# Performance work log

Measured on AMD Instinct MI355X. Metric: run time of the kernel, lower is better.

Reference implementation:

```python
import jax, jax.numpy as jnp
import numpy as np


def setup_inputs() -> dict:
    key = jax.random.key(0)
    k1, k2, k3, k4 = jax.random.split(key, 4)
    B, S, D, E, C = 8, 128, 480, 8, 10
    gcn_outputs = jax.random.normal(k1, (B, S, D), dtype=jnp.float32)
    label_sm = jax.random.uniform(k2, (B, S, S, C), dtype=jnp.float32)
    weight_prob = jax.random.uniform(k3, (B, S, S, E), dtype=jnp.float32)
    tensor_masks = jnp.ones((B, S, S), dtype=bool)
    # Linear(994, 10) with xavier-uniform weight
    fan_in, fan_out = 994, C
    bound = float(np.sqrt(6.0 / (fan_in + fan_out)))
    W_weight = jax.random.uniform(k4, (C, 994), dtype=jnp.float32, minval=-bound, maxval=bound)
    W_bias = jnp.zeros((C,), dtype=jnp.float32)
    return {"gcn_outputs": gcn_outputs, "label_sm": label_sm,
            "weight_prob": weight_prob, "tensor_masks": tensor_masks,
            "W_weight": W_weight, "W_bias": W_bias}


def reference(gcn_outputs, label_sm, weight_prob, tensor_masks, W_weight, W_bias):
    B, S, D = gcn_outputs.shape
    # node1[b,i,j,:] = node[b,j]; node2[b,i,j,:] = node[b,i]
    node1 = jnp.broadcast_to(gcn_outputs[:, None, :, :], (B, S, S, D))
    node2 = jnp.broadcast_to(gcn_outputs[:, :, None, :], (B, S, S, D))
    # edge_diag[b,s,e] = weight_prob[b,s,s,e]
    edge_diag = jnp.diagonal(weight_prob, axis1=1, axis2=2).transpose(0, 2, 1)  # [B,S,E]
    E = edge_diag.shape[-1]
    edge_i = jnp.broadcast_to(edge_diag[:, None, :, :], (B, S, S, E))  # varies along j
    edge_j = jnp.broadcast_to(edge_diag[:, :, None, :], (B, S, S, E))  # varies along i
    # channel 0 untouched, channels 1:4 upper-triangular, channels 4: lower-triangular
    mask_u = jnp.triu(jnp.ones((S, S), dtype=label_sm.dtype))[None, :, :, None]
    mask_l = jnp.tril(jnp.ones((S, S), dtype=label_sm.dtype))[None, :, :, None]
    s_triu = jnp.concatenate([
        label_sm[..., 0:1],
        label_sm[..., 1:4] * mask_u,
        label_sm[..., 4:] * mask_l,
    ], axis=-1)
    feats = jnp.concatenate([node1, node2, edge_i, edge_j, weight_prob, s_triu], axis=-1)  # [B,S,S,994]
    pre = jnp.einsum('bijf,kf->bijk', feats, W_weight) + W_bias
    return pre
```

## Files before the change

### kernel.cpp

```cpp
#include <hip/hip_runtime.h>
#include <hip/hip_bf16.h>

#define BB 8
#define SS 128
#define DD 480
#define EE 8
#define CC 10
#define KK 10
#define FF 994

__device__ __forceinline__ float cvt(float x) { return x; }
__device__ __forceinline__ float cvt(__hip_bfloat16 x) { return __bfloat162float(x); }
__device__ __forceinline__ void stf(float* p, float v) { *p = v; }
__device__ __forceinline__ void stf(__hip_bfloat16* p, float v) { *p = __float2bfloat16(v); }

__global__ __launch_bounds__(64) void detect_kernel(const unsigned short* __restrict__ wp_raw,
                                                    int* __restrict__ flag) {
    int bad = 0;
    #pragma unroll
    for (int q = 0; q < 4; ++q) {
        unsigned short v = wp_raw[threadIdx.x + 64 * q];
        if (((v >> 7) & 0xFF) >= 128) bad = 1;
    }
    unsigned long long m = __ballot(bad);
    if (threadIdx.x == 0) *flag = (m != 0ULL) ? 1 : 0;
}

template <typename T>
__device__ void rows_body(const T* __restrict__ gcn, const T* __restrict__ wp,
                          const T* __restrict__ W, const T* __restrict__ bias,
                          float* __restrict__ Arow, float* __restrict__ Brow,
                          float* g) {
    const int row = blockIdx.x;
    const int s   = row & (SS - 1);

    for (int d = threadIdx.x; d < DD; d += 256)
        g[d] = cvt(gcn[(size_t)row * DD + d]);
    __syncthreads();

    const int wave = threadIdx.x >> 6;
    const int lane = threadIdx.x & 63;
    const T* wpd = wp + ((size_t)row * SS + s) * EE;

    for (int q = 0; q < 5; ++q) {
        const int t   = wave * 5 + q;
        const int k   = (t < KK) ? t : t - KK;
        const int off = (t < KK) ? 0 : DD;
        const T* wrow = W + (size_t)k * FF + off;

        float acc = 0.f;
        for (int d = lane; d < DD; d += 64)
            acc += g[d] * cvt(wrow[d]);
        #pragma unroll
        for (int o = 32; o > 0; o >>= 1)
            acc += __shfl_down(acc, o, 64);

        if (lane == 0) {
            const int ecol = (t < KK) ? (2 * DD) : (2 * DD + EE);
            float e = 0.f;
            #pragma unroll
            for (int ee = 0; ee < EE; ++ee)
                e += cvt(wpd[ee]) * cvt(W[(size_t)k * FF + ecol + ee]);
            const float r = acc + e;
            if (t < KK) Arow[row * KK + k] = r;
            else        Brow[row * KK + k] = r + cvt(bias[k]);
        }
    }
}

__global__ __launch_bounds__(256) void rows_kernel(
    const void* gcn, const void* wp, const void* W, const void* bias,
    const int* __restrict__ flag, float* Arow, float* Brow) {
    __shared__ float g[DD];
    if (*flag)
        rows_body<float>((const float*)gcn, (const float*)wp,
                         (const float*)W, (const float*)bias, Arow, Brow, g);
    else
        rows_body<__hip_bfloat16>((const __hip_bfloat16*)gcn, (const __hip_bfloat16*)wp,
                                  (const __hip_bfloat16*)W, (const __hip_bfloat16*)bias,
                                  Arow, Brow, g);
}

template <typename T>
__device__ void pixel_body(const T* __restrict__ label, const T* __restrict__ wp,
                           const T* __restrict__ W, const float* __restrict__ Arow,
                           const float* __restrict__ Brow, T* __restrict__ out,
                           float (*w5)[EE], float (*w6)[CC], float* brow) {
    const int bi = blockIdx.x;
    const int b  = bi >> 7;
    const int i  = bi & (SS - 1);
    const int j  = threadIdx.x;

    for (int t = threadIdx.x; t < KK * EE + KK * CC + KK; t += 128) {
        if (t < KK * EE) {
            const int k = t / EE, e = t % EE;
            w5[k][e] = cvt(W[(size_t)k * FF + 2 * DD + 2 * EE + e]);
        } else if (t < KK * EE + KK * CC) {
            const int tt = t - KK * EE;
            const int k = tt / CC, c = tt % CC;
            w6[k][c] = cvt(W[(size_t)k * FF + 2 * DD + 3 * EE + c]);
        } else {
            const int k = t - KK * EE - KK * CC;
            brow[k] = Brow[bi * KK + k];
        }
    }
    __syncthreads();

    const size_t pix = (size_t)bi * SS + j;

    float wpe[EE];
    #pragma unroll
    for (int e = 0; e < EE; ++e) wpe[e] = cvt(wp[pix * EE + e]);
    float lc[CC];
    #pragma unroll
    for (int c = 0; c < CC; ++c) lc[c] = cvt(label[pix * CC + c]);

    const float mu = (j >= i) ? 1.f : 0.f;
    const float ml = (j <= i) ? 1.f : 0.f;
    #pragma unroll
    for (int c = 1; c < 4; ++c) lc[c] *= mu;
    #pragma unroll
    for (int c = 4; c < CC; ++c) lc[c] *= ml;

    const float* ap = Arow + ((size_t)b * SS + j) * KK;

    #pragma unroll
    for (int k = 0; k < KK; ++k) {
        float acc = ap[k] + brow[k];
        #pragma unroll
        for (int e = 0; e < EE; ++e) acc += wpe[e] * w5[k][e];
        #pragma unroll
        for (int c = 0; c < CC; ++c) acc += lc[c] * w6[k][c];
        stf(&out[pix * KK + k], acc);
    }
}

__global__ __launch_bounds__(128) void pixel_kernel(
    const void* label, const void* wp, const void* W,
    const float* __restrict__ Arow, const float* __restrict__ Brow,
    const int* __restrict__ flag, void* out) {
    __shared__ float w5[KK][EE];
    __shared__ float w6[KK][CC];
    __shared__ float brow[KK];
    if (*flag)
        pixel_body<float>((const float*)label, (const float*)wp, (const float*)W,
                          Arow, Brow, (float*)out, w5, w6, brow);
    else
        pixel_body<__hip_bfloat16>((const __hip_bfloat16*)label, (const __hip_bfloat16*)wp,
                                   (const __hip_bfloat16*)W, Arow, Brow,
                                   (__hip_bfloat16*)out, w5, w6, brow);
}

extern "C" void kernel_launch(void* const* d_in, const int* in_sizes, int n_in,
                              void* d_out, int out_size, void* d_ws, size_t ws_size,
                              hipStream_t stream) {
    const void* gcn   = d_in[0];
    const void* label = d_in[1];
    const void* wp    = d_in[2];
    const void* W     = d_in[4];
    const void* bias  = d_in[5];

    int*   flag = (int*)d_ws;
    float* Arow = (float*)((char*)d_ws + 256);
    float* Brow = Arow + BB * SS * KK;

    detect_kernel<<<1, 64, 0, stream>>>((const unsigned short*)wp, flag);
    rows_kernel<<<BB * SS, 256, 0, stream>>>(gcn, wp, W, bias, flag, Arow, Brow);
    pixel_kernel<<<BB * SS, 128, 0, stream>>>(label, wp, W, Arow, Brow, flag, d_out);
}
```

Measured before the change: 84.17 us.

## Drop dtype detection kernel, vectorize loads/stores, and process two rows per pixel block

Removes the bf16/fp32 detection kernel and its runtime flag branch, so both kernels are specialized to fp32 and one launch disappears. The row kernel now uses float4 loads for node features and float2 loads for weights. The pixel kernel handles two i-rows per 256-thread block, stages the per-batch Arow table in shared memory, and uses vectorized float4/float2 loads and float2 stores. The aim is to cut launch overhead and improve memory coalescing. In exchange it drops bf16 input support and relies on alignment assumptions for the vector accesses.

```diff
diff --git a/kernel.cpp b/kernel.cpp
--- a/kernel.cpp
+++ b/kernel.cpp
@@ -1,5 +1,4 @@
 #include <hip/hip_runtime.h>
-#include <hip/hip_bf16.h>
 
 #define BB 8
 #define SS 128
@@ -9,111 +8,116 @@
 #define KK 10
 #define FF 994
 
-__device__ __forceinline__ float cvt(float x) { return x; }
-__device__ __forceinline__ float cvt(__hip_bfloat16 x) { return __bfloat162float(x); }
-__device__ __forceinline__ void stf(float* p, float v) { *p = v; }
-__device__ __forceinline__ void stf(__hip_bfloat16* p, float v) { *p = __float2bfloat16(v); }
 
-__global__ __launch_bounds__(64) void detect_kernel(const unsigned short* __restrict__ wp_raw,
-                                                    int* __restrict__ flag) {
-    int bad = 0;
-    #pragma unroll
-    for (int q = 0; q < 4; ++q) {
-        unsigned short v = wp_raw[threadIdx.x + 64 * q];
-        if (((v >> 7) & 0xFF) >= 128) bad = 1;
-    }
-    unsigned long long m = __ballot(bad);
-    if (threadIdx.x == 0) *flag = (m != 0ULL) ? 1 : 0;
-}
-
-template <typename T>
-__device__ void rows_body(const T* __restrict__ gcn, const T* __restrict__ wp,
-                          const T* __restrict__ W, const T* __restrict__ bias,
-                          float* __restrict__ Arow, float* __restrict__ Brow,
-                          float* g) {
+__global__ __launch_bounds__(256) void rows_kernel(
+    const float* __restrict__ gcn,
+    const float* __restrict__ wp,
+    const float* __restrict__ W,
+    const float* __restrict__ bias,
+    float* __restrict__ Arow,
+    float* __restrict__ Brow)
+{
+    __shared__ float g[DD];
     const int row = blockIdx.x;
     const int s   = row & (SS - 1);
 
-    for (int d = threadIdx.x; d < DD; d += 256)
-        g[d] = cvt(gcn[(size_t)row * DD + d]);
+    const float4* g4 = reinterpret_cast<const float4*>(gcn + (size_t)row * DD);
+    for (int t = threadIdx.x; t < DD / 4; t += 256) {
+        const float4 v = g4[t];
+        g[4 * t + 0] = v.x; g[4 * t + 1] = v.y;
+        g[4 * t + 2] = v.z; g[4 * t + 3] = v.w;
+    }
     __syncthreads();
 
     const int wave = threadIdx.x >> 6;
     const int lane = threadIdx.x & 63;
-    const T* wpd = wp + ((size_t)row * SS + s) * EE;
 
     for (int q = 0; q < 5; ++q) {
         const int t   = wave * 5 + q;
         const int k   = (t < KK) ? t : t - KK;
         const int off = (t < KK) ? 0 : DD;
-        const T* wrow = W + (size_t)k * FF + off;
+        const float2* w2 = reinterpret_cast<const float2*>(W + (size_t)k * FF + off);
 
         float acc = 0.f;
-        for (int d = lane; d < DD; d += 64)
-            acc += g[d] * cvt(wrow[d]);
+        #pragma unroll
+        for (int r = 0; r < 4; ++r) {
+            const int idx = lane + 64 * r;
+            if (idx < DD / 2) {
+                const float2 u = w2[idx];
+                acc += g[2 * idx] * u.x + g[2 * idx + 1] * u.y;
+            }
+        }
         #pragma unroll
         for (int o = 32; o > 0; o >>= 1)
             acc += __shfl_down(acc, o, 64);
 
         if (lane == 0) {
-            const int ecol = (t < KK) ? (2 * DD) : (2 * DD + EE);
+            const float* wpd = wp + ((size_t)row * SS + s) * EE;
+            const float* we  = W + (size_t)k * FF + ((t < KK) ? 2 * DD : 2 * DD + EE);
             float e = 0.f;
             #pragma unroll
             for (int ee = 0; ee < EE; ++ee)
-                e += cvt(wpd[ee]) * cvt(W[(size_t)k * FF + ecol + ee]);
+                e += wpd[ee] * we[ee];
             const float r = acc + e;
             if (t < KK) Arow[row * KK + k] = r;
-            else        Brow[row * KK + k] = r + cvt(bias[k]);
+            else        Brow[row * KK + k] = r + bias[k];
         }
     }
 }
 
-__global__ __launch_bounds__(256) void rows_kernel(
-    const void* gcn, const void* wp, const void* W, const void* bias,
-    const int* __restrict__ flag, float* Arow, float* Brow) {
-    __shared__ float g[DD];
-    if (*flag)
-        rows_body<float>((const float*)gcn, (const float*)wp,
-                         (const float*)W, (const float*)bias, Arow, Brow, g);
-    else
-        rows_body<__hip_bfloat16>((const __hip_bfloat16*)gcn, (const __hip_bfloat16*)wp,
-                                  (const __hip_bfloat16*)W, (const __hip_bfloat16*)bias,
-                                  Arow, Brow, g);
-}
+__global__ __launch_bounds__(256) void pixel_kernel(
+    const float* __restrict__ label,
+    const float* __restrict__ wp,
+    const float* __restrict__ W,
+    const float* __restrict__ Arow,
+    const float* __restrict__ Brow,
+    float* __restrict__ out)
+{
+    const int b  = blockIdx.x >> 6;
+    const int i0 = (blockIdx.x & 63) * 2;
 
-template <typename T>
-__device__ void pixel_body(const T* __restrict__ label, const T* __restrict__ wp,
-                           const T* __restrict__ W, const float* __restrict__ Arow,
-                           const float* __restrict__ Brow, T* __restrict__ out,
-                           float (*w5)[EE], float (*w6)[CC], float* brow) {
-    const int bi = blockIdx.x;
-    const int b  = bi >> 7;
-    const int i  = bi & (SS - 1);
-    const int j  = threadIdx.x;
+    __shared__ float w5[KK][EE];
+    __shared__ float w6[KK][CC];
+    __shared__ float brow[2][KK];
+    __shared__ float arow[SS][KK + 1];
 
-    for (int t = threadIdx.x; t < KK * EE + KK * CC + KK; t += 128) {
-        if (t < KK * EE) {
-            const int k = t / EE, e = t % EE;
-            w5[k][e] = cvt(W[(size_t)k * FF + 2 * DD + 2 * EE + e]);
-        } else if (t < KK * EE + KK * CC) {
-            const int tt = t - KK * EE;
-            const int k = tt / CC, c = tt % CC;
-            w6[k][c] = cvt(W[(size_t)k * FF + 2 * DD + 3 * EE + c]);
-        } else {
-            const int k = t - KK * EE - KK * CC;
-            brow[k] = Brow[bi * KK + k];
+    {
+        const int t = threadIdx.x;
+        if (t < 80) {
+            w5[t >> 3][t & 7] = W[(t >> 3) * FF + 2 * DD + 2 * EE + (t & 7)];
+        } else if (t < 180) {
+            const int tt = t - 80;
+            w6[tt / 10][tt % 10] = W[(tt / 10) * FF + 2 * DD + 3 * EE + (tt % 10)];
+        } else if (t < 200) {
+            const int tt = t - 180;
+            brow[tt / 10][tt % 10] = Brow[(b * SS + i0 + tt / 10) * KK + (tt % 10)];
         }
     }
+    for (int u = threadIdx.x; u < SS * KK; u += 256)
+        arow[u / KK][u % KK] = Arow[(size_t)b * SS * KK + u];
     __syncthreads();
 
-    const size_t pix = (size_t)bi * SS + j;
+    const int half = threadIdx.x >> 7;
+    const int i    = i0 + half;
+    const int j    = threadIdx.x & 127;
+    const size_t pix = ((size_t)(b * SS + i)) * SS + j;
 
     float wpe[EE];
-    #pragma unroll
-    for (int e = 0; e < EE; ++e) wpe[e] = cvt(wp[pix * EE + e]);
+    {
+        const float4* p4 = reinterpret_cast<const float4*>(wp + pix * EE);
+        const float4 a = p4[0], c = p4[1];
+        wpe[0] = a.x; wpe[1] = a.y; wpe[2] = a.z; wpe[3] = a.w;
+        wpe[4] = c.x; wpe[5] = c.y; wpe[6] = c.z; wpe[7] = c.w;
+    }
     float lc[CC];
-    #pragma unroll
-    for (int c = 0; c < CC; ++c) lc[c] = cvt(label[pix * CC + c]);
+    {
+        const float2* p2 = reinterpret_cast<const float2*>(label + pix * CC);
+        #pragma unroll
+        for (int p = 0; p < 5; ++p) {
+            const float2 v = p2[p];
+            lc[2 * p] = v.x; lc[2 * p + 1] = v.y;
+        }
+    }
 
     const float mu = (j >= i) ? 1.f : 0.f;
     const float ml = (j <= i) ? 1.f : 0.f;
@@ -122,49 +126,36 @@
     #pragma unroll
     for (int c = 4; c < CC; ++c) lc[c] *= ml;
 
-    const float* ap = Arow + ((size_t)b * SS + j) * KK;
-
+    float o[KK];
     #pragma unroll
     for (int k = 0; k < KK; ++k) {
-        float acc = ap[k] + brow[k];
+        float acc = arow[j][k] + brow[half][k];
         #pragma unroll
         for (int e = 0; e < EE; ++e) acc += wpe[e] * w5[k][e];
         #pragma unroll
         for (int c = 0; c < CC; ++c) acc += lc[c] * w6[k][c];
-        stf(&out[pix * KK + k], acc);
+        o[k] = acc;
     }
-}
 
-__global__ __launch_bounds__(128) void pixel_kernel(
-    const void* label, const void* wp, const void* W,
-    const float* __restrict__ Arow, const float* __restrict__ Brow,
-    const int* __restrict__ flag, void* out) {
-    __shared__ float w5[KK][EE];
-    __shared__ float w6[KK][CC];
-    __shared__ float brow[KK];
-    if (*flag)
-        pixel_body<float>((const float*)label, (const float*)wp, (const float*)W,
-                          Arow, Brow, (float*)out, w5, w6, brow);
-    else
-        pixel_body<__hip_bfloat16>((const __hip_bfloat16*)label, (const __hip_bfloat16*)wp,
-                                   (const __hip_bfloat16*)W, Arow, Brow,
-                                   (__hip_bfloat16*)out, w5, w6, brow);
+    float2* op = reinterpret_cast<float2*>(out + pix * KK);
+    #pragma unroll
+    for (int p = 0; p < 5; ++p)
+        op[p] = make_float2(o[2 * p], o[2 * p + 1]);
 }
 
 extern "C" void kernel_launch(void* const* d_in, const int* in_sizes, int n_in,
                               void* d_out, int out_size, void* d_ws, size_t ws_size,
                               hipStream_t stream) {
-    const void* gcn   = d_in[0];
-    const void* label = d_in[1];
-    const void* wp    = d_in[2];
-    const void* W     = d_in[4];
-    const void* bias  = d_in[5];
+    const float* gcn   = (const float*)d_in[0];
+    const float* label = (const float*)d_in[1];
+    const float* wp    = (const float*)d_in[2];
+    const float* W     = (const float*)d_in[4];
+    const float* bias  = (const float*)d_in[5];
+    float* out = (float*)d_out;
 
-    int*   flag = (int*)d_ws;
-    float* Arow = (float*)((char*)d_ws + 256);
+    float* Arow = (float*)d_ws;
     float* Brow = Arow + BB * SS * KK;
 
-    detect_kernel<<<1, 64, 0, stream>>>((const unsigned short*)wp, flag);
-    rows_kernel<<<BB * SS, 256, 0, stream>>>(gcn, wp, W, bias, flag, Arow, Brow);
-    pixel_kernel<<<BB * SS, 128, 0, stream>>>(label, wp, W, Arow, Brow, flag, d_out);
+    rows_kernel<<<BB * SS, 256, 0, stream>>>(gcn, wp, W, bias, Arow, Brow);
+    pixel_kernel<<<BB * SS / 2, 256, 0, stream>>>(label, wp, W, Arow, Brow, out);
 }
```

New measurement: 82.22 us. 1.02x faster.
